# Performance work log

Measured on AMD Instinct MI355X. Metric: run time of the kernel, lower is better.

## Reference

```python
import jax, jax.numpy as jnp
import numpy as np

B, S, D_MODEL, D_OUT = 8, 2048, 1024, 64

def setup_inputs() -> dict:
    key = jax.random.key(0)
    ks = jax.random.split(key, 9)
    scale = 1.0 / np.sqrt(D_MODEL)
    q = jax.random.normal(ks[0], (B, S, D_MODEL), dtype=jnp.float32)
    k = jax.random.normal(ks[1], (B, S, D_MODEL), dtype=jnp.float32)
    v = jax.random.normal(ks[2], (B, S, D_MODEL), dtype=jnp.float32)
    # causal mask: 1 where attending allowed, 0 where blocked
    mask = jnp.tril(jnp.ones((S, S), dtype=jnp.int32))[None, :, :]  # [1,S,S]
    Wq = jax.random.normal(ks[3], (D_MODEL, D_OUT), dtype=jnp.float32) * scale
    Wk = jax.random.normal(ks[4], (D_MODEL, D_OUT), dtype=jnp.float32) * scale
    Wv = jax.random.normal(ks[5], (D_MODEL, D_OUT), dtype=jnp.float32) * scale
    bq = jnp.zeros((D_OUT,), dtype=jnp.float32)
    bk = jnp.zeros((D_OUT,), dtype=jnp.float32)
    bv = jnp.zeros((D_OUT,), dtype=jnp.float32)
    return {"q": q, "k": k, "v": v, "mask": mask,
            "Wq": Wq, "bq": bq, "Wk": Wk, "bk": bk, "Wv": Wv, "bv": bv}

def reference(q, k, v, mask, Wq, bq, Wk, bk, Wv, bv):
    # projections: [B,S,d_model] @ [d_model,d_out] + bias
    query = jnp.einsum('bsd,df->bsf', q, Wq) + bq
    key_ = jnp.einsum('bsd,df->bsf', k, Wk) + bk
    value = jnp.einsum('bsd,df->bsf', v, Wv) + bv
    dim_k = key_.shape[-1]
    scores = jnp.einsum('bqf,bkf->bqk', query, key_) / jnp.sqrt(jnp.float32(dim_k))
    scores = jnp.where(mask == 0, -jnp.inf, scores)
    weights = jax.nn.softmax(scores, axis=-1)  # dropout p=0 (eval)
    outputs = jnp.einsum('bqk,bkf->bqf', weights, value)
    return outputs
```

## Files before the change

kernel.cpp:

```cpp
#include <hip/hip_runtime.h>


#define DM 1024
#define DO 64
#define SQ 2048

typedef __attribute__((ext_vector_type(4))) float f32x4;
typedef __attribute__((ext_vector_type(8))) short bf16x8;

__device__ __forceinline__ short f2bf(float x) {
  union { float f; unsigned u; } v; v.f = x;
  unsigned r = v.u + 0x7FFFu + ((v.u >> 16) & 1u);
  return (short)(r >> 16);
}

__global__ __launch_bounds__(256) void k_wconv(const float* __restrict__ Wq,
                                               const float* __restrict__ Wk,
                                               const float* __restrict__ Wv,
                                               short* __restrict__ Wt) {
  int id = blockIdx.x * 256 + threadIdx.x;
  int m = id >> 16;
  int rem = id & 65535;
  int cidx = rem >> 10;
  int kk = rem & 1023;
  const float* W = (m == 0) ? Wq : (m == 1) ? Wk : Wv;
  Wt[id] = f2bf(W[kk * DO + cidx]);
}

__global__ __launch_bounds__(256) void k_proj(const float* __restrict__ q,
                                              const float* __restrict__ k,
                                              const float* __restrict__ v,
                                              const float* __restrict__ bq,
                                              const float* __restrict__ bk,
                                              const float* __restrict__ bv,
                                              const short* __restrict__ Wt,
                                              short* __restrict__ Qp,
                                              short* __restrict__ Kp,
                                              short* __restrict__ Vt) {
  int bid = blockIdx.x;
  int m = bid >> 8, mt = bid & 255;
  const float* X    = (m == 0) ? q  : (m == 1) ? k  : v;
  const float* bias = (m == 0) ? bq : (m == 1) ? bk : bv;
  const short* W = Wt + (m << 16);
  int tid = threadIdx.x;
  int w = tid >> 6, lane = tid & 63, g = lane >> 4, c = lane & 15;
  const float* Xrow = X + (size_t)(mt * 64 + 16 * w + c) * DM;
  f32x4 acc[4] = {{0,0,0,0},{0,0,0,0},{0,0,0,0},{0,0,0,0}};
#pragma unroll 4
  for (int k0 = 0; k0 < DM; k0 += 32) {
    const float* xp = Xrow + k0 + 8 * g;
    f32x4 xa = *(const f32x4*)xp;
    f32x4 xb = *(const f32x4*)(xp + 4);
    bf16x8 af;
    af[0] = f2bf(xa[0]); af[1] = f2bf(xa[1]); af[2] = f2bf(xa[2]); af[3] = f2bf(xa[3]);
    af[4] = f2bf(xb[0]); af[5] = f2bf(xb[1]); af[6] = f2bf(xb[2]); af[7] = f2bf(xb[3]);
#pragma unroll
    for (int ct = 0; ct < 4; ++ct) {
      bf16x8 bfr = *(const bf16x8*)(W + (16 * ct + c) * DM + k0 + 8 * g);
      acc[ct] = __builtin_amdgcn_mfma_f32_16x16x32_bf16(af, bfr, acc[ct], 0, 0, 0);
    }
  }
  int row0 = mt * 64 + 16 * w;
  if (m < 2) {
    short* dst = (m == 0) ? Qp : Kp;
#pragma unroll
    for (int ct = 0; ct < 4; ++ct) {
      float bb = bias[16 * ct + c];
#pragma unroll
      for (int r = 0; r < 4; ++r)
        dst[(size_t)(row0 + 4 * g + r) * DO + 16 * ct + c] = f2bf(acc[ct][r] + bb);
    }
  } else {
    int batch = row0 >> 11, sl = row0 & 2047;
#pragma unroll
    for (int ct = 0; ct < 4; ++ct) {
      float bb = bias[16 * ct + c];
      ushort4 pk;
      pk.x = (unsigned short)f2bf(acc[ct][0] + bb);
      pk.y = (unsigned short)f2bf(acc[ct][1] + bb);
      pk.z = (unsigned short)f2bf(acc[ct][2] + bb);
      pk.w = (unsigned short)f2bf(acc[ct][3] + bb);
      *(ushort4*)(Vt + (size_t)(batch * 64 + 16 * ct + c) * SQ + sl + 4 * g) = pk;
    }
  }
}

__device__ __forceinline__ void attn_task(int batch, int t, int k0, int kend, int slot,
                                          int g, int c, short (*P)[72],
                                          const short* __restrict__ Qp,
                                          const short* __restrict__ Kp,
                                          const short* __restrict__ Vt,
                                          float* __restrict__ Po,
                                          float* __restrict__ Pml) {
  const int qb = t * 16;
  const short* Qrow = Qp + (size_t)((batch << 11) + qb + c) * DO;
  bf16x8 qf0 = *(const bf16x8*)(Qrow + 8 * g);
  bf16x8 qf1 = *(const bf16x8*)(Qrow + 32 + 8 * g);
  f32x4 acc[4] = {{0,0,0,0},{0,0,0,0},{0,0,0,0},{0,0,0,0}};
  float mr[4] = {-1e30f, -1e30f, -1e30f, -1e30f};
  float lr[4] = {0.f, 0.f, 0.f, 0.f};
  int nkt = (kend - k0 + 63) >> 6;
  for (int kt = 0; kt < nkt; ++kt) {
    int kk = k0 + (kt << 6);
    f32x4 s[4];
#pragma unroll
    for (int ct = 0; ct < 4; ++ct) {
      const short* Krow = Kp + (size_t)((batch << 11) + kk + 16 * ct + c) * DO;
      bf16x8 kf0 = *(const bf16x8*)(Krow + 8 * g);
      bf16x8 kf1 = *(const bf16x8*)(Krow + 32 + 8 * g);
      f32x4 z = {0, 0, 0, 0};
      z = __builtin_amdgcn_mfma_f32_16x16x32_bf16(qf0, kf0, z, 0, 0, 0);
      z = __builtin_amdgcn_mfma_f32_16x16x32_bf16(qf1, kf1, z, 0, 0, 0);
      s[ct] = z;
    }
#pragma unroll
    for (int ct = 0; ct < 4; ++ct) {
      int col = kk + 16 * ct + c;
#pragma unroll
      for (int r = 0; r < 4; ++r) {
        float vv = s[ct][r] * 0.125f;
        if (col > qb + 4 * g + r) vv = -1e30f;
        s[ct][r] = vv;
      }
    }
#pragma unroll
    for (int r = 0; r < 4; ++r) {
      float rm = fmaxf(fmaxf(s[0][r], s[1][r]), fmaxf(s[2][r], s[3][r]));
      rm = fmaxf(rm, __shfl_xor(rm, 1));
      rm = fmaxf(rm, __shfl_xor(rm, 2));
      rm = fmaxf(rm, __shfl_xor(rm, 4));
      rm = fmaxf(rm, __shfl_xor(rm, 8));
      float mnew = fmaxf(mr[r], rm);
      float sf = __expf(mr[r] - mnew);
      mr[r] = mnew;
      float rs = 0.f;
#pragma unroll
      for (int ct = 0; ct < 4; ++ct) {
        float p = __expf(s[ct][r] - mnew);
        s[ct][r] = p;
        rs += p;
      }
      rs += __shfl_xor(rs, 1);
      rs += __shfl_xor(rs, 2);
      rs += __shfl_xor(rs, 4);
      rs += __shfl_xor(rs, 8);
      lr[r] = lr[r] * sf + rs;
#pragma unroll
      for (int dt = 0; dt < 4; ++dt) acc[dt][r] *= sf;
    }
#pragma unroll
    for (int ct = 0; ct < 4; ++ct)
#pragma unroll
      for (int r = 0; r < 4; ++r)
        P[4 * g + r][16 * ct + c] = f2bf(s[ct][r]);
#pragma unroll
    for (int ks = 0; ks < 2; ++ks) {
      bf16x8 pf = *(const bf16x8*)&P[c][32 * ks + 8 * g];
#pragma unroll
      for (int dt = 0; dt < 4; ++dt) {
        const short* Vr = Vt + (size_t)(batch * 64 + 16 * dt + c) * SQ + kk + 32 * ks + 8 * g;
        bf16x8 vf = *(const bf16x8*)Vr;
        acc[dt] = __builtin_amdgcn_mfma_f32_16x16x32_bf16(pf, vf, acc[dt], 0, 0, 0);
      }
    }
  }
  float* Pb = Po + ((size_t)((batch * 128 + t) * 4 + slot) << 10);
#pragma unroll
  for (int dt = 0; dt < 4; ++dt)
#pragma unroll
    for (int r = 0; r < 4; ++r)
      Pb[(4 * g + r) * 64 + 16 * dt + c] = acc[dt][r];
  if (c == 0) {
    float* Mb = Pml + ((size_t)((batch * 128 + t) * 4 + slot) << 5);
#pragma unroll
    for (int r = 0; r < 4; ++r) {
      Mb[(4 * g + r) * 2]     = mr[r];
      Mb[(4 * g + r) * 2 + 1] = lr[r];
    }
  }
}

__global__ __launch_bounds__(256) void k_attn(const short* __restrict__ Qp,
                                              const short* __restrict__ Kp,
                                              const short* __restrict__ Vt,
                                              float* __restrict__ Po,
                                              float* __restrict__ Pml) {
  __shared__ __align__(16) short Plds[4][16][72];
  int tid = threadIdx.x;
  int w = tid >> 6, lane = tid & 63, g = lane >> 4, c = lane & 15;
  short (*P)[72] = Plds[w];
  int task = blockIdx.x * 4 + w;
  int batch = task / 260;
  int tau = task - batch * 260;
  int tA, k0A, keA, slA;
  int tB = -1, k0B = 0, keB = 0, slB = 0;
  if (tau < 196) {
    int ch, t;
    if (tau < 97)       { ch = 0; t = 31 + tau; }
    else if (tau < 162) { ch = 1; t = 63 + (tau - 97); }
    else if (tau < 195) { ch = 2; t = 95 + (tau - 162); }
    else                { ch = 3; t = 127; }
    tA = t; k0A = 512 * ch; keA = 512 * (ch + 1); slA = ch;
  } else {
    int u = tau - 196;
    int base = (u >> 4) * 32, j = u & 15;
    int t1 = base + j, t2 = base + 30 - j;
    tA = t1; k0A = 512 * (t1 >> 5); keA = 16 * t1 + 16; slA = t1 >> 5;
    if (t2 != t1) { tB = t2; k0B = 512 * (t2 >> 5); keB = 16 * t2 + 16; slB = t2 >> 5; }
  }
  attn_task(batch, tA, k0A, keA, slA, g, c, P, Qp, Kp, Vt, Po, Pml);
  if (tB >= 0)
    attn_task(batch, tB, k0B, keB, slB, g, c, P, Qp, Kp, Vt, Po, Pml);
}

__global__ __launch_bounds__(256) void k_combine(const float* __restrict__ Po,
                                                 const float* __restrict__ Pml,
                                                 float* __restrict__ out) {
  int id = blockIdx.x * 256 + threadIdx.x;
  int d4  = id & 15;
  int row = (id >> 4) & 15;
  int t   = (id >> 8) & 127;
  int b   = id >> 15;
  int nch = (t >> 5) + 1;
  size_t base = (size_t)(b * 128 + t) * 4;
  float mv[4], lv[4];
  float m = -1e30f;
  for (int ci = 0; ci < nch; ++ci) {
    const float* ml = Pml + ((base + ci) << 5) + row * 2;
    mv[ci] = ml[0];
    lv[ci] = ml[1];
    m = fmaxf(m, mv[ci]);
  }
  float lsum = 0.f;
  f32x4 o = {0, 0, 0, 0};
  for (int ci = 0; ci < nch; ++ci) {
    float e = __expf(mv[ci] - m);
    lsum += lv[ci] * e;
    f32x4 oc = *(const f32x4*)(Po + ((base + ci) << 10) + row * 64 + d4 * 4);
    o[0] += oc[0] * e; o[1] += oc[1] * e; o[2] += oc[2] * e; o[3] += oc[3] * e;
  }
  float inv = 1.0f / lsum;
  f32x4 res = {o[0] * inv, o[1] * inv, o[2] * inv, o[3] * inv};
  *(f32x4*)(out + (size_t)((b * 2048 + t * 16 + row) * 64) + d4 * 4) = res;
}

extern "C" void kernel_launch(void* const* d_in, const int* in_sizes, int n_in,
                              void* d_out, int out_size, void* d_ws, size_t ws_size,
                              hipStream_t stream) {
  const float* q  = (const float*)d_in[0];
  const float* k  = (const float*)d_in[1];
  const float* v  = (const float*)d_in[2];
  const float* Wq = (const float*)d_in[4];
  const float* bq = (const float*)d_in[5];
  const float* Wk = (const float*)d_in[6];
  const float* bk = (const float*)d_in[7];
  const float* Wv = (const float*)d_in[8];
  const float* bv = (const float*)d_in[9];

  char* ws = (char*)d_ws;
  short* Wt  = (short*)(ws);
  short* Qp  = (short*)(ws + 393216);
  short* Kp  = (short*)(ws + 2490368);
  short* Vt  = (short*)(ws + 4587520);
  float* Po  = (float*)(ws + 6684672);
  float* Pml = (float*)(ws + 23461888);
  float* out = (float*)d_out;

  hipLaunchKernelGGL(k_wconv,   dim3(768),  dim3(256), 0, stream, Wq, Wk, Wv, Wt);
  hipLaunchKernelGGL(k_proj,    dim3(768),  dim3(256), 0, stream, q, k, v, bq, bk, bv, Wt, Qp, Kp, Vt);
  hipLaunchKernelGGL(k_attn,    dim3(520),  dim3(256), 0, stream, Qp, Kp, Vt, Po, Pml);
  hipLaunchKernelGGL(k_combine, dim3(1024), dim3(256), 0, stream, Po, Pml, out);
}
```

Before: 294.4 us.

## Repartition projection with split-K, finer attention chunks, LDS-transposed weight conversion

Weight conversion now transposes through an LDS tile so both reads and writes are coalesced. The projection kernel uses 16-row tiles split across two waves along K, with register prefetch of X and an LDS reduction, giving more blocks for occupancy. Attention switches to 256-key chunks indexed by a triangular schedule, 576 tasks per batch, and the V fragments are loaded before the softmax so that load latency overlaps it. The change adds more partial results for combine to merge and more synchronisation.

```diff
diff --git a/kernel.cpp b/kernel.cpp
--- a/kernel.cpp
+++ b/kernel.cpp
@@ -18,16 +18,27 @@
                                                const float* __restrict__ Wk,
                                                const float* __restrict__ Wv,
                                                short* __restrict__ Wt) {
-  int id = blockIdx.x * 256 + threadIdx.x;
-  int m = id >> 16;
-  int rem = id & 65535;
-  int cidx = rem >> 10;
-  int kk = rem & 1023;
+  __shared__ short tile[64][65];
+  int bid = blockIdx.x;
+  int m = bid >> 4, ti = bid & 15;
   const float* W = (m == 0) ? Wq : (m == 1) ? Wk : Wv;
-  Wt[id] = f2bf(W[kk * DO + cidx]);
-}
-
-__global__ __launch_bounds__(256) void k_proj(const float* __restrict__ q,
+  int tid = threadIdx.x;
+#pragma unroll
+  for (int i = 0; i < 16; ++i) {
+    int lin = tid + 256 * i;
+    int r = lin >> 6, cc = lin & 63;
+    tile[r][cc] = f2bf(W[(ti * 64 + r) * 64 + cc]);
+  }
+  __syncthreads();
+#pragma unroll
+  for (int i = 0; i < 16; ++i) {
+    int lin = tid + 256 * i;
+    int cc = lin >> 6, r = lin & 63;
+    Wt[(m << 16) + cc * DM + ti * 64 + r] = tile[r][cc];
+  }
+}
+
+__global__ __launch_bounds__(128) void k_proj(const float* __restrict__ q,
                                               const float* __restrict__ k,
                                               const float* __restrict__ v,
                                               const float* __restrict__ bq,
@@ -37,61 +48,87 @@
                                               short* __restrict__ Qp,
                                               short* __restrict__ Kp,
                                               short* __restrict__ Vt) {
+  __shared__ float red[2][16][64];
   int bid = blockIdx.x;
-  int m = bid >> 8, mt = bid & 255;
+  int m = bid >> 10, mt = bid & 1023;
   const float* X    = (m == 0) ? q  : (m == 1) ? k  : v;
   const float* bias = (m == 0) ? bq : (m == 1) ? bk : bv;
   const short* W = Wt + (m << 16);
   int tid = threadIdx.x;
   int w = tid >> 6, lane = tid & 63, g = lane >> 4, c = lane & 15;
-  const float* Xrow = X + (size_t)(mt * 64 + 16 * w + c) * DM;
+  const float* Xrow = X + (size_t)(mt * 16 + c) * DM + (w << 9);
+  const short* Wc = W + (w << 9);
+
+  f32x4 pa[4], pb[4];
+#pragma unroll
+  for (int i = 0; i < 4; ++i) {
+    const float* xp = Xrow + 32 * i + 8 * g;
+    pa[i] = *(const f32x4*)xp;
+    pb[i] = *(const f32x4*)(xp + 4);
+  }
   f32x4 acc[4] = {{0,0,0,0},{0,0,0,0},{0,0,0,0},{0,0,0,0}};
-#pragma unroll 4
-  for (int k0 = 0; k0 < DM; k0 += 32) {
-    const float* xp = Xrow + k0 + 8 * g;
-    f32x4 xa = *(const f32x4*)xp;
-    f32x4 xb = *(const f32x4*)(xp + 4);
+#pragma unroll
+  for (int i = 0; i < 16; ++i) {
+    f32x4 xa = pa[i & 3], xb = pb[i & 3];
+    if (i < 12) {
+      const float* xp = Xrow + 32 * (i + 4) + 8 * g;
+      pa[i & 3] = *(const f32x4*)xp;
+      pb[i & 3] = *(const f32x4*)(xp + 4);
+    }
     bf16x8 af;
     af[0] = f2bf(xa[0]); af[1] = f2bf(xa[1]); af[2] = f2bf(xa[2]); af[3] = f2bf(xa[3]);
     af[4] = f2bf(xb[0]); af[5] = f2bf(xb[1]); af[6] = f2bf(xb[2]); af[7] = f2bf(xb[3]);
+    int k0 = 32 * i;
 #pragma unroll
     for (int ct = 0; ct < 4; ++ct) {
-      bf16x8 bfr = *(const bf16x8*)(W + (16 * ct + c) * DM + k0 + 8 * g);
+      bf16x8 bfr = *(const bf16x8*)(Wc + (16 * ct + c) * DM + k0 + 8 * g);
       acc[ct] = __builtin_amdgcn_mfma_f32_16x16x32_bf16(af, bfr, acc[ct], 0, 0, 0);
     }
   }
-  int row0 = mt * 64 + 16 * w;
+#pragma unroll
+  for (int ct = 0; ct < 4; ++ct)
+#pragma unroll
+    for (int r = 0; r < 4; ++r)
+      red[w][4 * g + r][16 * ct + c] = acc[ct][r];
+  __syncthreads();
+
+  int row0 = mt * 16;
   if (m < 2) {
     short* dst = (m == 0) ? Qp : Kp;
-#pragma unroll
-    for (int ct = 0; ct < 4; ++ct) {
-      float bb = bias[16 * ct + c];
-#pragma unroll
-      for (int r = 0; r < 4; ++r)
-        dst[(size_t)(row0 + 4 * g + r) * DO + 16 * ct + c] = f2bf(acc[ct][r] + bb);
+    int col = tid & 63, rb = (tid >> 6) * 8;
+#pragma unroll
+    for (int rr = 0; rr < 8; ++rr) {
+      int r = rb + rr;
+      float vsum = red[0][r][col] + red[1][r][col] + bias[col];
+      dst[(size_t)(row0 + r) * DO + col] = f2bf(vsum);
     }
   } else {
-    int batch = row0 >> 11, sl = row0 & 2047;
-#pragma unroll
-    for (int ct = 0; ct < 4; ++ct) {
-      float bb = bias[16 * ct + c];
-      ushort4 pk;
-      pk.x = (unsigned short)f2bf(acc[ct][0] + bb);
-      pk.y = (unsigned short)f2bf(acc[ct][1] + bb);
-      pk.z = (unsigned short)f2bf(acc[ct][2] + bb);
-      pk.w = (unsigned short)f2bf(acc[ct][3] + bb);
-      *(ushort4*)(Vt + (size_t)(batch * 64 + 16 * ct + c) * SQ + sl + 4 * g) = pk;
-    }
-  }
-}
-
-__device__ __forceinline__ void attn_task(int batch, int t, int k0, int kend, int slot,
+    int col = tid >> 1, rb = (tid & 1) * 8;
+    int batch = mt >> 7;
+    int s0 = ((mt & 127) << 4) + rb;
+    float bb = bias[col];
+    float vv[8];
+#pragma unroll
+    for (int rr = 0; rr < 8; ++rr)
+      vv[rr] = red[0][rb + rr][col] + red[1][rb + rr][col] + bb;
+    ushort4 p0, p1;
+    p0.x = (unsigned short)f2bf(vv[0]); p0.y = (unsigned short)f2bf(vv[1]);
+    p0.z = (unsigned short)f2bf(vv[2]); p0.w = (unsigned short)f2bf(vv[3]);
+    p1.x = (unsigned short)f2bf(vv[4]); p1.y = (unsigned short)f2bf(vv[5]);
+    p1.z = (unsigned short)f2bf(vv[6]); p1.w = (unsigned short)f2bf(vv[7]);
+    short* Vb = Vt + (size_t)(batch * 64 + col) * SQ + s0;
+    *(ushort4*)Vb = p0;
+    *(ushort4*)(Vb + 4) = p1;
+  }
+}
+
+__device__ __forceinline__ void attn_task(int batch, int t, int k0, int kend,
                                           int g, int c, short (*P)[72],
                                           const short* __restrict__ Qp,
                                           const short* __restrict__ Kp,
                                           const short* __restrict__ Vt,
-                                          float* __restrict__ Po,
-                                          float* __restrict__ Pml) {
+                                          float* __restrict__ Pb,
+                                          float* __restrict__ Mb) {
   const int qb = t * 16;
   const short* Qrow = Qp + (size_t)((batch << 11) + qb + c) * DO;
   bf16x8 qf0 = *(const bf16x8*)(Qrow + 8 * g);
@@ -113,6 +150,13 @@
       z = __builtin_amdgcn_mfma_f32_16x16x32_bf16(qf1, kf1, z, 0, 0, 0);
       s[ct] = z;
     }
+    bf16x8 vf[8];
+#pragma unroll
+    for (int ks = 0; ks < 2; ++ks)
+#pragma unroll
+      for (int dt = 0; dt < 4; ++dt)
+        vf[ks * 4 + dt] = *(const bf16x8*)(Vt + (size_t)(batch * 64 + 16 * dt + c) * SQ
+                                           + kk + 32 * ks + 8 * g);
 #pragma unroll
     for (int ct = 0; ct < 4; ++ct) {
       int col = kk + 16 * ct + c;
@@ -157,21 +201,16 @@
     for (int ks = 0; ks < 2; ++ks) {
       bf16x8 pf = *(const bf16x8*)&P[c][32 * ks + 8 * g];
 #pragma unroll
-      for (int dt = 0; dt < 4; ++dt) {
-        const short* Vr = Vt + (size_t)(batch * 64 + 16 * dt + c) * SQ + kk + 32 * ks + 8 * g;
-        bf16x8 vf = *(const bf16x8*)Vr;
-        acc[dt] = __builtin_amdgcn_mfma_f32_16x16x32_bf16(pf, vf, acc[dt], 0, 0, 0);
-      }
-    }
-  }
-  float* Pb = Po + ((size_t)((batch * 128 + t) * 4 + slot) << 10);
+      for (int dt = 0; dt < 4; ++dt)
+        acc[dt] = __builtin_amdgcn_mfma_f32_16x16x32_bf16(pf, vf[ks * 4 + dt], acc[dt], 0, 0, 0);
+    }
+  }
 #pragma unroll
   for (int dt = 0; dt < 4; ++dt)
 #pragma unroll
     for (int r = 0; r < 4; ++r)
       Pb[(4 * g + r) * 64 + 16 * dt + c] = acc[dt][r];
   if (c == 0) {
-    float* Mb = Pml + ((size_t)((batch * 128 + t) * 4 + slot) << 5);
 #pragma unroll
     for (int r = 0; r < 4; ++r) {
       Mb[(4 * g + r) * 2]     = mr[r];
@@ -188,29 +227,21 @@
   __shared__ __align__(16) short Plds[4][16][72];
   int tid = threadIdx.x;
   int w = tid >> 6, lane = tid & 63, g = lane >> 4, c = lane & 15;
-  short (*P)[72] = Plds[w];
   int task = blockIdx.x * 4 + w;
-  int batch = task / 260;
-  int tau = task - batch * 260;
-  int tA, k0A, keA, slA;
-  int tB = -1, k0B = 0, keB = 0, slB = 0;
-  if (tau < 196) {
-    int ch, t;
-    if (tau < 97)       { ch = 0; t = 31 + tau; }
-    else if (tau < 162) { ch = 1; t = 63 + (tau - 97); }
-    else if (tau < 195) { ch = 2; t = 95 + (tau - 162); }
-    else                { ch = 3; t = 127; }
-    tA = t; k0A = 512 * ch; keA = 512 * (ch + 1); slA = ch;
-  } else {
-    int u = tau - 196;
-    int base = (u >> 4) * 32, j = u & 15;
-    int t1 = base + j, t2 = base + 30 - j;
-    tA = t1; k0A = 512 * (t1 >> 5); keA = 16 * t1 + 16; slA = t1 >> 5;
-    if (t2 != t1) { tB = t2; k0B = 512 * (t2 >> 5); keB = 16 * t2 + 16; slB = t2 >> 5; }
-  }
-  attn_task(batch, tA, k0A, keA, slA, g, c, P, Qp, Kp, Vt, Po, Pml);
-  if (tB >= 0)
-    attn_task(batch, tB, k0B, keB, slB, g, c, P, Qp, Kp, Vt, Po, Pml);
+  int batch = task / 576;
+  int idx = task - batch * 576;
+  int o = (int)((sqrtf(1.0f + 0.5f * (float)idx) - 1.0f) * 0.5f);
+  while (8 * (o + 1) * (o + 2) <= idx) ++o;
+  while (8 * o * (o + 1) > idx) --o;
+  int rem = idx - 8 * o * (o + 1);
+  int j = rem / (o + 1);
+  int ch = rem - j * (o + 1);
+  int t = 16 * o + j;
+  int k0 = ch << 8;
+  int kend = min(k0 + 256, 16 * t + 16);
+  float* Pb = Po + ((size_t)task << 10);
+  float* Mb = Pml + ((size_t)task << 5);
+  attn_task(batch, t, k0, kend, g, c, Plds[w], Qp, Kp, Vt, Pb, Mb);
 }
 
 __global__ __launch_bounds__(256) void k_combine(const float* __restrict__ Po,
@@ -221,27 +252,25 @@
   int row = (id >> 4) & 15;
   int t   = (id >> 8) & 127;
   int b   = id >> 15;
-  int nch = (t >> 5) + 1;
-  size_t base = (size_t)(b * 128 + t) * 4;
-  float mv[4], lv[4];
+  int o = t >> 4, j = t & 15;
+  int nch = o + 1;
+  size_t sbase = (size_t)b * 576 + 8 * o * (o + 1) + j * (o + 1);
   float m = -1e30f;
+  for (int ci = 0; ci < nch; ++ci)
+    m = fmaxf(m, Pml[((sbase + ci) << 5) + row * 2]);
+  float lsum = 0.f;
+  f32x4 oacc = {0, 0, 0, 0};
   for (int ci = 0; ci < nch; ++ci) {
-    const float* ml = Pml + ((base + ci) << 5) + row * 2;
-    mv[ci] = ml[0];
-    lv[ci] = ml[1];
-    m = fmaxf(m, mv[ci]);
-  }
-  float lsum = 0.f;
-  f32x4 o = {0, 0, 0, 0};
-  for (int ci = 0; ci < nch; ++ci) {
-    float e = __expf(mv[ci] - m);
-    lsum += lv[ci] * e;
-    f32x4 oc = *(const f32x4*)(Po + ((base + ci) << 10) + row * 64 + d4 * 4);
-    o[0] += oc[0] * e; o[1] += oc[1] * e; o[2] += oc[2] * e; o[3] += oc[3] * e;
+    const float* ml = Pml + ((sbase + ci) << 5) + row * 2;
+    float e = __expf(ml[0] - m);
+    lsum += ml[1] * e;
+    f32x4 oc = *(const f32x4*)(Po + ((sbase + ci) << 10) + row * 64 + d4 * 4);
+    oacc[0] += oc[0] * e; oacc[1] += oc[1] * e;
+    oacc[2] += oc[2] * e; oacc[3] += oc[3] * e;
   }
   float inv = 1.0f / lsum;
-  f32x4 res = {o[0] * inv, o[1] * inv, o[2] * inv, o[3] * inv};
-  *(f32x4*)(out + (size_t)((b * 2048 + t * 16 + row) * 64) + d4 * 4) = res;
+  f32x4 res = {oacc[0] * inv, oacc[1] * inv, oacc[2] * inv, oacc[3] * inv};
+  *(f32x4*)(out + (size_t)((b << 11) + (t << 4) + row) * 64 + d4 * 4) = res;
 }
 
 extern "C" void kernel_launch(void* const* d_in, const int* in_sizes, int n_in,
@@ -263,11 +292,11 @@
   short* Kp  = (short*)(ws + 2490368);
   short* Vt  = (short*)(ws + 4587520);
   float* Po  = (float*)(ws + 6684672);
-  float* Pml = (float*)(ws + 23461888);
+  float* Pml = (float*)(ws + 25559040);
   float* out = (float*)d_out;
 
-  hipLaunchKernelGGL(k_wconv,   dim3(768),  dim3(256), 0, stream, Wq, Wk, Wv, Wt);
-  hipLaunchKernelGGL(k_proj,    dim3(768),  dim3(256), 0, stream, q, k, v, bq, bk, bv, Wt, Qp, Kp, Vt);
-  hipLaunchKernelGGL(k_attn,    dim3(520),  dim3(256), 0, stream, Qp, Kp, Vt, Po, Pml);
+  hipLaunchKernelGGL(k_wconv,   dim3(48),   dim3(256), 0, stream, Wq, Wk, Wv, Wt);
+  hipLaunchKernelGGL(k_proj,    dim3(3072), dim3(128), 0, stream, q, k, v, bq, bk, bv, Wt, Qp, Kp, Vt);
+  hipLaunchKernelGGL(k_attn,    dim3(1152), dim3(256), 0, stream, Qp, Kp, Vt, Po, Pml);
   hipLaunchKernelGGL(k_combine, dim3(1024), dim3(256), 0, stream, Po, Pml, out);
 }
```

Result: no change. 289.2 us (-1.8%).
